# Optimization experiments

Measured on AMD Instinct MI355X. Metric: run time of the kernel, lower is better.

The kernel has to match this reference:

```python
import jax, jax.numpy as jnp
import numpy as np

N, M, C = 32768, 8192, 128
K = 3            # number of interpolation neighbors (PointNet++/RepSurf FP)
EPS_BN = 1e-5    # torch BatchNorm1d default eps
EPS_D = 1e-8     # RepSurf dist_recip eps


def setup_inputs() -> dict:
    key = jax.random.key(0)
    ks = jax.random.split(key, 16)
    s = 0.05
    inp = {
        "pos1": jax.random.normal(ks[0], (N, 3), jnp.float32),
        "pos2": jax.random.normal(ks[1], (M, 3), jnp.float32),
        "feat2": jax.random.normal(ks[2], (M, C), jnp.float32),
    }
    # MLP stack [128,128,128]: Linear + BatchNorm1d (gamma/beta) per layer
    for i in range(3):
        inp[f"W{i}"] = jax.random.normal(ks[3 + i], (C, C), jnp.float32) * s
        inp[f"b{i}"] = jnp.zeros((C,), jnp.float32)
        inp[f"g{i}"] = jnp.ones((C,), jnp.float32)
        inp[f"be{i}"] = jnp.zeros((C,), jnp.float32)
    return inp


def _lin_bn_relu(x, W, b, g, be):
    # Linear -> BatchNorm1d (training-mode batch stats, biased var) -> ReLU
    y = x @ W.T + b
    m = y.mean(axis=0)
    v = y.var(axis=0)
    return jax.nn.relu((y - m) * jax.lax.rsqrt(v + EPS_BN) * g + be)


def reference(pos1, pos2, feat2, W0, b0, g0, be0, W1, b1, g1, be1, W2, b2, g2, be2):
    # squared pairwise distances [N, M] (memory-bound: 1 GB fp32)
    d = ((pos1 ** 2).sum(-1, keepdims=True)
         + (pos2 ** 2).sum(-1)[None, :]
         - 2.0 * (pos1 @ pos2.T))
    neg_d, idx = jax.lax.top_k(-d, K)          # 3 nearest neighbors
    dk = jnp.maximum(-neg_d, 0.0)              # [N, K] squared dists
    w = 1.0 / (dk + EPS_D)
    w = w / w.sum(-1, keepdims=True)           # inverse-distance weights
    # gather neighbor features and interpolate: [N, K, C] -> [N, C]
    interp = jnp.einsum('nkc,nk->nc', feat2[idx], w)
    x = _lin_bn_relu(interp, W0, b0, g0, be0)
    x = _lin_bn_relu(x, W1, b1, g1, be1)
    x = _lin_bn_relu(x, W2, b2, g2, be2)
    return x
```

## Files before the change

### kernel.cpp

```cpp
#include <hip/hip_runtime.h>
#include <math.h>

#define NQ 32768
#define MC 8192
#define CC 128
#define EPS_BN 1e-5f
#define EPS_D  1e-8

#define DBL_BIG 1e300
#define IDX_BIG 0x7fffffff

#define QB  64
#define TB  512
#define NW  8
#define CH  2048
#define HM  (MC / 2)
#define NCH (HM / CH)
#define SLC (CH / NW)
#define KMASK 0xFFFFE000u
#define IMASK 0x1FFFu
#define NSURV 64

typedef __attribute__((ext_vector_type(8))) short bf16x8;
typedef __attribute__((ext_vector_type(4))) float floatx4;
typedef unsigned short ushort_t;

__device__ __forceinline__ unsigned umin_(unsigned a, unsigned b) { return a < b ? a : b; }
__device__ __forceinline__ unsigned umax_(unsigned a, unsigned b) { return a > b ? a : b; }

__device__ __forceinline__ unsigned bf16pair(float a, float b) {
    unsigned ua = __float_as_uint(a); ua = (ua + 0x7FFFu + ((ua >> 16) & 1u)) >> 16;
    unsigned ub = __float_as_uint(b); ub = (ub + 0x7FFFu + ((ub >> 16) & 1u)) >> 16;
    return ua | (ub << 16);
}

__global__ __launch_bounds__(TB) void knn_kernel(const float* __restrict__ pos1,
                                                 const float* __restrict__ pos2,
                                                 unsigned* __restrict__ skeys) {
    __shared__ float4 sp4[CH * 3 / 4];
    __shared__ unsigned skey[QB][NW * 4];

    const int half = blockIdx.x & 1;
    const int bq   = blockIdx.x >> 1;
    const int wv = threadIdx.x >> 6;
    const int ln = threadIdx.x & 63;
    const int q  = bq * QB + ln;

    const float px = pos1[q * 3 + 0];
    const float py = pos1[q * 3 + 1];
    const float pz = pos1[q * 3 + 2];

    unsigned k0 = 0xFFFFFFFFu, k1 = 0xFFFFFFFFu, k2 = 0xFFFFFFFFu, k3 = 0xFFFFFFFFu;

    for (int c0 = 0; c0 < NCH; ++c0) {
        const int cb = half * HM + c0 * CH;
        __syncthreads();
        {
            const float4* g4 = (const float4*)(pos2 + (size_t)cb * 3);
#pragma unroll
            for (int i = threadIdx.x; i < CH * 3 / 4; i += TB) sp4[i] = g4[i];
        }
        __syncthreads();
        const float4* b4 = sp4 + wv * (SLC * 3 / 4);
        const int jb = cb + wv * SLC;
#pragma unroll 2
        for (int gi = 0; gi < SLC / 4; ++gi) {
            const float4 A = b4[gi * 3 + 0];
            const float4 B = b4[gi * 3 + 1];
            const float4 Cv = b4[gi * 3 + 2];
            const int j = jb + gi * 4;
            const float cx[4] = {A.x, A.w, B.z, Cv.y};
            const float cy[4] = {A.y, B.x, B.w, Cv.z};
            const float cz[4] = {A.z, B.y, Cv.x, Cv.w};
#pragma unroll
            for (int u = 0; u < 4; ++u) {
                const float dx = px - cx[u], dy = py - cy[u], dz = pz - cz[u];
                const float d = fmaf(dx, dx, fmaf(dy, dy, dz * dz));
                unsigned e = (__float_as_uint(d) & KMASK) | (unsigned)(j + u);
                unsigned t;
                t = umin_(k0, e); e = umax_(k0, e); k0 = t;
                t = umin_(k1, e); e = umax_(k1, e); k1 = t;
                t = umin_(k2, e); e = umax_(k2, e); k2 = t;
                k3 = umin_(k3, e);
            }
        }
    }
    skey[ln][wv * 4 + 0] = k0;
    skey[ln][wv * 4 + 1] = k1;
    skey[ln][wv * 4 + 2] = k2;
    skey[ln][wv * 4 + 3] = k3;
    __syncthreads();

#pragma unroll
    for (int t = threadIdx.x * 4; t < threadIdx.x * 4 + 4; ++t) {
        const int ql = t >> 5, slot = t & 31;
        skeys[(size_t)((bq * QB + ql) * 2 + half) * 32 + slot] = skey[ql][slot];
    }
}

__global__ __launch_bounds__(256) void rerank_kernel(const float* __restrict__ pos1,
                                                     const float* __restrict__ pos2,
                                                     const unsigned* __restrict__ skeys,
                                                     int* __restrict__ idx3,
                                                     float* __restrict__ w3) {
    const int q = blockIdx.x * 256 + threadIdx.x;
    const double qx = (double)pos1[q * 3 + 0];
    const double qy = (double)pos1[q * 3 + 1];
    const double qz = (double)pos1[q * 3 + 2];
    double b0 = DBL_BIG, b1 = DBL_BIG, b2 = DBL_BIG;
    int    j0 = IDX_BIG, j1 = IDX_BIG, j2 = IDX_BIG;
    const uint4* kp = (const uint4*)(skeys + (size_t)q * NSURV);
#pragma unroll 4
    for (int g = 0; g < NSURV / 4; ++g) {
        const uint4 kk = kp[g];
        const unsigned ks[4] = {kk.x, kk.y, kk.z, kk.w};
#pragma unroll
        for (int u = 0; u < 4; ++u) {
            const int id = (int)(ks[u] & IMASK);
            const double x = (double)pos2[id * 3 + 0];
            const double y = (double)pos2[id * 3 + 1];
            const double z = (double)pos2[id * 3 + 2];
            const double ax = qx - x, ay = qy - y, az = qz - z;
            const double d = ax * ax + ay * ay + az * az;
            const bool l2 = (d < b2) || (d == b2 && id < j2);
            if (l2) {
                const bool l1 = (d < b1) || (d == b1 && id < j1);
                const bool l0 = (d < b0) || (d == b0 && id < j0);
                b2 = l1 ? b1 : d;              j2 = l1 ? j1 : id;
                b1 = l1 ? (l0 ? b0 : d) : b1;  j1 = l1 ? (l0 ? j0 : id) : j1;
                b0 = l0 ? d : b0;              j0 = l0 ? id : j0;
            }
        }
    }
    const double r0 = 1.0 / (fmax(b0, 0.0) + EPS_D);
    const double r1 = 1.0 / (fmax(b1, 0.0) + EPS_D);
    const double r2 = 1.0 / (fmax(b2, 0.0) + EPS_D);
    const double inv = 1.0 / (r0 + r1 + r2);
    idx3[q * 3 + 0] = j0; idx3[q * 3 + 1] = j1; idx3[q * 3 + 2] = j2;
    w3[q * 3 + 0] = (float)(r0 * inv);
    w3[q * 3 + 1] = (float)(r1 * inv);
    w3[q * 3 + 2] = (float)(r2 * inv);
}

__global__ __launch_bounds__(256) void prep_w(const float* __restrict__ W0,
                                              const float* __restrict__ W1,
                                              const float* __restrict__ W2,
                                              ushort_t* __restrict__ out) {
    const int l = blockIdx.x >> 4;
    const int i4 = ((blockIdx.x & 15) * 256 + threadIdx.x) * 4;
    const float* W = (l == 0) ? W0 : ((l == 1) ? W1 : W2);
    const float4 v = *(const float4*)&W[i4];
    unsigned* dst = (unsigned*)(out + (size_t)l * CC * CC);
    dst[(i4 >> 1) + 0] = bf16pair(v.x, v.y);
    dst[(i4 >> 1) + 1] = bf16pair(v.z, v.w);
}

template <int MODE>
__global__ __launch_bounds__(256) void gemm_mfma(const float* __restrict__ Xsrc,
                                                 const int* __restrict__ idx3,
                                                 const float* __restrict__ w3,
                                                 const float* __restrict__ scale,
                                                 const float* __restrict__ shift,
                                                 const ushort_t* __restrict__ Wb,
                                                 const float* __restrict__ bias,
                                                 float* __restrict__ Y,
                                                 float* __restrict__ partials) {
    __shared__ short xa[64][136];
    __shared__ short wb[128][136];
    __shared__ float blk_s[CC], blk_q[CC];

    const int row0 = blockIdx.x * 64;

    if (threadIdx.x < CC) { blk_s[threadIdx.x] = 0.f; blk_q[threadIdx.x] = 0.f; }

#pragma unroll
    for (int e = threadIdx.x; e < 64 * 32; e += 256) {
        const int r = e >> 5, c4 = e & 31;
        const int nrow = row0 + r;
        float4 v;
        if (MODE == 0) {
            const int i0 = idx3[nrow * 3 + 0], i1 = idx3[nrow * 3 + 1], i2 = idx3[nrow * 3 + 2];
            const float w0 = w3[nrow * 3 + 0], w1 = w3[nrow * 3 + 1], w2 = w3[nrow * 3 + 2];
            const float4 f0 = *(const float4*)&Xsrc[(size_t)i0 * CC + c4 * 4];
            const float4 f1 = *(const float4*)&Xsrc[(size_t)i1 * CC + c4 * 4];
            const float4 f2 = *(const float4*)&Xsrc[(size_t)i2 * CC + c4 * 4];
            v.x = w0 * f0.x + w1 * f1.x + w2 * f2.x;
            v.y = w0 * f0.y + w1 * f1.y + w2 * f2.y;
            v.z = w0 * f0.z + w1 * f1.z + w2 * f2.z;
            v.w = w0 * f0.w + w1 * f1.w + w2 * f2.w;
        } else {
            const float4 x  = *(const float4*)&Xsrc[(size_t)nrow * CC + c4 * 4];
            const float4 sc = *(const float4*)&scale[c4 * 4];
            const float4 sh = *(const float4*)&shift[c4 * 4];
            v.x = fmaxf(fmaf(x.x, sc.x, sh.x), 0.f);
            v.y = fmaxf(fmaf(x.y, sc.y, sh.y), 0.f);
            v.z = fmaxf(fmaf(x.z, sc.z, sh.z), 0.f);
            v.w = fmaxf(fmaf(x.w, sc.w, sh.w), 0.f);
        }
        unsigned* dst = (unsigned*)&xa[r][0];
        dst[c4 * 2 + 0] = bf16pair(v.x, v.y);
        dst[c4 * 2 + 1] = bf16pair(v.z, v.w);
    }
#pragma unroll
    for (int e = threadIdx.x; e < 128 * 16; e += 256) {
        const int co = e >> 4, seg = e & 15;
        *(float4*)&wb[co][seg * 8] = *(const float4*)&Wb[(size_t)co * CC + seg * 8];
    }
    __syncthreads();

    const int lane = threadIdx.x & 63;
    const int wv = threadIdx.x >> 6;
    const int nn = lane & 15;
    const int quad = lane >> 4;

    floatx4 acc[8] = {};

    const short* arow = &xa[wv * 16 + nn][0];
#pragma unroll
    for (int ks = 0; ks < 4; ++ks) {
        const bf16x8 a = *(const bf16x8*)(arow + ks * 32 + quad * 8);
#pragma unroll
        for (int ct = 0; ct < 8; ++ct) {
            const bf16x8 b = *(const bf16x8*)(&wb[ct * 16 + nn][0] + ks * 32 + quad * 8);
            acc[ct] = __builtin_amdgcn_mfma_f32_16x16x32_bf16(a, b, acc[ct], 0, 0, 0);
        }
    }

#pragma unroll
    for (int ct = 0; ct < 8; ++ct) {
        const float bv = bias[ct * 16 + nn];
        float s = 0.f, qv = 0.f;
#pragma unroll
        for (int r = 0; r < 4; ++r) {
            acc[ct][r] += bv;
            s += acc[ct][r];
            qv = fmaf(acc[ct][r], acc[ct][r], qv);
        }
#pragma unroll
        for (int r = 0; r < 4; ++r)
            Y[(size_t)(row0 + wv * 16 + quad * 4 + r) * CC + ct * 16 + nn] = acc[ct][r];
        s += __shfl_xor(s, 16, 64); s += __shfl_xor(s, 32, 64);
        qv += __shfl_xor(qv, 16, 64); qv += __shfl_xor(qv, 32, 64);
        if (quad == 0) {
            atomicAdd(&blk_s[ct * 16 + nn], s);
            atomicAdd(&blk_q[ct * 16 + nn], qv);
        }
    }
    __syncthreads();
    {
        const int ch = threadIdx.x;
        const float v = (ch < CC) ? blk_s[ch] : blk_q[ch - CC];
        partials[(size_t)ch * 512 + blockIdx.x] = v;
    }
}

__global__ __launch_bounds__(256) void reduce_stats(const float* __restrict__ P,
                                                    const float* __restrict__ g,
                                                    const float* __restrict__ be,
                                                    float* __restrict__ sc,
                                                    float* __restrict__ sh) {
    __shared__ float accS[4], accQ[4];
    const int c = blockIdx.x;
    const int t = threadIdx.x;
    float s  = P[(size_t)c * 512 + t]        + P[(size_t)c * 512 + 256 + t];
    float qv = P[(size_t)(c + CC) * 512 + t] + P[(size_t)(c + CC) * 512 + 256 + t];
#pragma unroll
    for (int off = 32; off >= 1; off >>= 1) {
        s  += __shfl_xor(s, off, 64);
        qv += __shfl_xor(qv, off, 64);
    }
    if ((t & 63) == 0) { accS[t >> 6] = s; accQ[t >> 6] = qv; }
    __syncthreads();
    if (t == 0) {
        const float S = accS[0] + accS[1] + accS[2] + accS[3];
        const float Q = accQ[0] + accQ[1] + accQ[2] + accQ[3];
        const float m = S * (1.f / (float)NQ);
        const float v = fmaf(-m, m, Q * (1.f / (float)NQ));
        const float rstd = rsqrtf(v + EPS_BN);
        const float scl = g[c] * rstd;
        sc[c] = scl;
        sh[c] = fmaf(-m, scl, be[c]);
    }
}

__global__ __launch_bounds__(256) void bn_relu_kernel(const float* __restrict__ Y,
                                                      const float* __restrict__ sc,
                                                      const float* __restrict__ sh,
                                                      float* __restrict__ out) {
    const int i4 = blockIdx.x * 256 + threadIdx.x;
    const int c4 = (i4 & 31) * 4;
    const float4 y = ((const float4*)Y)[i4];
    const float4 s = *(const float4*)&sc[c4];
    const float4 h = *(const float4*)&sh[c4];
    float4 o;
    o.x = fmaxf(fmaf(y.x, s.x, h.x), 0.f);
    o.y = fmaxf(fmaf(y.y, s.y, h.y), 0.f);
    o.z = fmaxf(fmaf(y.z, s.z, h.z), 0.f);
    o.w = fmaxf(fmaf(y.w, s.w, h.w), 0.f);
    ((float4*)out)[i4] = o;
}

extern "C" void kernel_launch(void* const* d_in, const int* in_sizes, int n_in,
                              void* d_out, int out_size, void* d_ws, size_t ws_size,
                              hipStream_t stream) {
    (void)in_sizes; (void)n_in; (void)out_size; (void)ws_size;

    const float* pos1  = (const float*)d_in[0];
    const float* pos2  = (const float*)d_in[1];
    const float* feat2 = (const float*)d_in[2];
    const float* Wl[3]  = {(const float*)d_in[3], (const float*)d_in[7],  (const float*)d_in[11]};
    const float* bl[3]  = {(const float*)d_in[4], (const float*)d_in[8],  (const float*)d_in[12]};
    const float* gl[3]  = {(const float*)d_in[5], (const float*)d_in[9],  (const float*)d_in[13]};
    const float* bel[3] = {(const float*)d_in[6], (const float*)d_in[10], (const float*)d_in[14]};

    float* ws = (float*)d_ws;
    float* B0   = ws;
    float* B1   = B0 + (size_t)NQ * CC;
    unsigned* skeys = (unsigned*)B1;
    int*   idx3 = (int*)(B1 + (size_t)NQ * CC);
    float* w3   = (float*)(idx3 + (size_t)NQ * 3);
    float* part = w3 + (size_t)NQ * 3;
    float* scsh = part + 256 * 512;
    ushort_t* Wbf = (ushort_t*)(scsh + 3 * 256);

    float* sc0 = scsh + 0 * 256; float* sh0 = sc0 + CC;
    float* sc1 = scsh + 1 * 256; float* sh1 = sc1 + CC;
    float* sc2 = scsh + 2 * 256; float* sh2 = sc2 + CC;

    prep_w<<<48, 256, 0, stream>>>(Wl[0], Wl[1], Wl[2], Wbf);
    knn_kernel<<<(NQ / QB) * 2, TB, 0, stream>>>(pos1, pos2, skeys);
    rerank_kernel<<<NQ / 256, 256, 0, stream>>>(pos1, pos2, skeys, idx3, w3);

    gemm_mfma<0><<<NQ / 64, 256, 0, stream>>>(feat2, idx3, w3, nullptr, nullptr,
                                              Wbf + 0 * CC * CC, bl[0], B0, part);
    reduce_stats<<<CC, 256, 0, stream>>>(part, gl[0], bel[0], sc0, sh0);
    gemm_mfma<1><<<NQ / 64, 256, 0, stream>>>(B0, nullptr, nullptr, sc0, sh0,
                                              Wbf + 1 * CC * CC, bl[1], B1, part);
    reduce_stats<<<CC, 256, 0, stream>>>(part, gl[1], bel[1], sc1, sh1);
    gemm_mfma<1><<<NQ / 64, 256, 0, stream>>>(B1, nullptr, nullptr, sc1, sh1,
                                              Wbf + 2 * CC * CC, bl[2], B0, part);
    reduce_stats<<<CC, 256, 0, stream>>>(part, gl[2], bel[2], sc2, sh2);
    bn_relu_kernel<<<(size_t)NQ * CC / 1024, 256, 0, stream>>>(B0, sc2, sh2, (float*)d_out);
}
```

Baseline: 231.7 us.

## Fuse weight prep, rerank and BN stats reduction into KNN and GEMM kernels

Weight bf16 conversion now runs in extra blocks of the KNN kernel. The distance loop uses an expanded form, with per-point squared norms precomputed into LDS as float4. The exact double-precision rerank moves into the first GEMM kernel, with four threads per query and an LDS merge. The separate reduce_stats kernels are replaced by a last-block-done atomic counter inside each GEMM, cutting the launch count roughly in half. The expanded float distance can cancel to small negative values that sort as huge keys, which risks dropping true neighbors in the coarse filter.

Measured after the change: 442.2 us. +90.9%, slower.

```diff
diff --git a/kernel.cpp b/kernel.cpp
--- a/kernel.cpp
+++ b/kernel.cpp
@@ -20,6 +20,8 @@
 #define KMASK 0xFFFFE000u
 #define IMASK 0x1FFFu
 #define NSURV 64
+#define KNN_B ((NQ / QB) * 2)
+#define GEMM_B (NQ / 64)
 
 typedef __attribute__((ext_vector_type(8))) short bf16x8;
 typedef __attribute__((ext_vector_type(4))) float floatx4;
@@ -36,9 +38,29 @@
 
 __global__ __launch_bounds__(TB) void knn_kernel(const float* __restrict__ pos1,
                                                  const float* __restrict__ pos2,
-                                                 unsigned* __restrict__ skeys) {
-    __shared__ float4 sp4[CH * 3 / 4];
+                                                 unsigned* __restrict__ skeys,
+                                                 const float* __restrict__ W0,
+                                                 const float* __restrict__ W1,
+                                                 const float* __restrict__ W2,
+                                                 ushort_t* __restrict__ Wbf,
+                                                 unsigned* __restrict__ cnt) {
+    __shared__ __align__(16) float4 sp4[CH];
     __shared__ unsigned skey[QB][NW * 4];
+
+    if (blockIdx.x >= KNN_B) {
+        const int pb = blockIdx.x - KNN_B;
+        const int f = pb * TB + threadIdx.x;
+        const float* Ws[3] = {W0, W1, W2};
+#pragma unroll
+        for (int l = 0; l < 3; ++l) {
+            const float4 v = ((const float4*)Ws[l])[f];
+            unsigned* dst = (unsigned*)(Wbf + (size_t)l * CC * CC);
+            dst[f * 2 + 0] = bf16pair(v.x, v.y);
+            dst[f * 2 + 1] = bf16pair(v.z, v.w);
+        }
+        if (pb == 0 && threadIdx.x < 4) cnt[threadIdx.x] = 0u;
+        return;
+    }
 
     const int half = blockIdx.x & 1;
     const int bq   = blockIdx.x >> 1;
@@ -49,6 +71,8 @@
     const float px = pos1[q * 3 + 0];
     const float py = pos1[q * 3 + 1];
     const float pz = pos1[q * 3 + 2];
+    const float s1 = px * px + py * py + pz * pz;
+    const float m2x = -2.f * px, m2y = -2.f * py, m2z = -2.f * pz;
 
     unsigned k0 = 0xFFFFFFFFu, k1 = 0xFFFFFFFFu, k2 = 0xFFFFFFFFu, k3 = 0xFFFFFFFFu;
 
@@ -56,33 +80,30 @@
         const int cb = half * HM + c0 * CH;
         __syncthreads();
         {
-            const float4* g4 = (const float4*)(pos2 + (size_t)cb * 3);
-#pragma unroll
-            for (int i = threadIdx.x; i < CH * 3 / 4; i += TB) sp4[i] = g4[i];
+            const float4* g = (const float4*)(pos2 + (size_t)(cb + threadIdx.x * 4) * 3);
+            const float4 f0 = g[0], f1 = g[1], f2 = g[2];
+            sp4[threadIdx.x * 4 + 0] = make_float4(f0.x, f0.y, f0.z,
+                fmaf(f0.x, f0.x, fmaf(f0.y, f0.y, f0.z * f0.z)));
+            sp4[threadIdx.x * 4 + 1] = make_float4(f0.w, f1.x, f1.y,
+                fmaf(f0.w, f0.w, fmaf(f1.x, f1.x, f1.y * f1.y)));
+            sp4[threadIdx.x * 4 + 2] = make_float4(f1.z, f1.w, f2.x,
+                fmaf(f1.z, f1.z, fmaf(f1.w, f1.w, f2.x * f2.x)));
+            sp4[threadIdx.x * 4 + 3] = make_float4(f2.y, f2.z, f2.w,
+                fmaf(f2.y, f2.y, fmaf(f2.z, f2.z, f2.w * f2.w)));
         }
         __syncthreads();
-        const float4* b4 = sp4 + wv * (SLC * 3 / 4);
+        const float4* b4 = sp4 + wv * SLC;
         const int jb = cb + wv * SLC;
-#pragma unroll 2
-        for (int gi = 0; gi < SLC / 4; ++gi) {
-            const float4 A = b4[gi * 3 + 0];
-            const float4 B = b4[gi * 3 + 1];
-            const float4 Cv = b4[gi * 3 + 2];
-            const int j = jb + gi * 4;
-            const float cx[4] = {A.x, A.w, B.z, Cv.y};
-            const float cy[4] = {A.y, B.x, B.w, Cv.z};
-            const float cz[4] = {A.z, B.y, Cv.x, Cv.w};
-#pragma unroll
-            for (int u = 0; u < 4; ++u) {
-                const float dx = px - cx[u], dy = py - cy[u], dz = pz - cz[u];
-                const float d = fmaf(dx, dx, fmaf(dy, dy, dz * dz));
-                unsigned e = (__float_as_uint(d) & KMASK) | (unsigned)(j + u);
-                unsigned t;
-                t = umin_(k0, e); e = umax_(k0, e); k0 = t;
-                t = umin_(k1, e); e = umax_(k1, e); k1 = t;
-                t = umin_(k2, e); e = umax_(k2, e); k2 = t;
-                k3 = umin_(k3, e);
-            }
+#pragma unroll 4
+        for (int e = 0; e < SLC; ++e) {
+            const float4 c = b4[e];
+            const float d = fmaf(m2x, c.x, fmaf(m2y, c.y, fmaf(m2z, c.z, c.w + s1)));
+            unsigned ek = (__float_as_uint(d) & KMASK) | (unsigned)(jb + e);
+            unsigned t;
+            t = umin_(k0, ek); ek = umax_(k0, ek); k0 = t;
+            t = umin_(k1, ek); ek = umax_(k1, ek); k1 = t;
+            t = umin_(k2, ek); ek = umax_(k2, ek); k2 = t;
+            k3 = umin_(k3, ek);
         }
     }
     skey[ln][wv * 4 + 0] = k0;
@@ -94,112 +115,138 @@
 #pragma unroll
     for (int t = threadIdx.x * 4; t < threadIdx.x * 4 + 4; ++t) {
         const int ql = t >> 5, slot = t & 31;
-        skeys[(size_t)((bq * QB + ql) * 2 + half) * 32 + slot] = skey[ql][slot];
-    }
-}
-
-__global__ __launch_bounds__(256) void rerank_kernel(const float* __restrict__ pos1,
-                                                     const float* __restrict__ pos2,
-                                                     const unsigned* __restrict__ skeys,
-                                                     int* __restrict__ idx3,
-                                                     float* __restrict__ w3) {
-    const int q = blockIdx.x * 256 + threadIdx.x;
-    const double qx = (double)pos1[q * 3 + 0];
-    const double qy = (double)pos1[q * 3 + 1];
-    const double qz = (double)pos1[q * 3 + 2];
-    double b0 = DBL_BIG, b1 = DBL_BIG, b2 = DBL_BIG;
-    int    j0 = IDX_BIG, j1 = IDX_BIG, j2 = IDX_BIG;
-    const uint4* kp = (const uint4*)(skeys + (size_t)q * NSURV);
-#pragma unroll 4
-    for (int g = 0; g < NSURV / 4; ++g) {
-        const uint4 kk = kp[g];
-        const unsigned ks[4] = {kk.x, kk.y, kk.z, kk.w};
-#pragma unroll
-        for (int u = 0; u < 4; ++u) {
-            const int id = (int)(ks[u] & IMASK);
-            const double x = (double)pos2[id * 3 + 0];
-            const double y = (double)pos2[id * 3 + 1];
-            const double z = (double)pos2[id * 3 + 2];
-            const double ax = qx - x, ay = qy - y, az = qz - z;
-            const double d = ax * ax + ay * ay + az * az;
-            const bool l2 = (d < b2) || (d == b2 && id < j2);
-            if (l2) {
-                const bool l1 = (d < b1) || (d == b1 && id < j1);
-                const bool l0 = (d < b0) || (d == b0 && id < j0);
-                b2 = l1 ? b1 : d;              j2 = l1 ? j1 : id;
-                b1 = l1 ? (l0 ? b0 : d) : b1;  j1 = l1 ? (l0 ? j0 : id) : j1;
-                b0 = l0 ? d : b0;              j0 = l0 ? id : j0;
-            }
-        }
-    }
-    const double r0 = 1.0 / (fmax(b0, 0.0) + EPS_D);
-    const double r1 = 1.0 / (fmax(b1, 0.0) + EPS_D);
-    const double r2 = 1.0 / (fmax(b2, 0.0) + EPS_D);
-    const double inv = 1.0 / (r0 + r1 + r2);
-    idx3[q * 3 + 0] = j0; idx3[q * 3 + 1] = j1; idx3[q * 3 + 2] = j2;
-    w3[q * 3 + 0] = (float)(r0 * inv);
-    w3[q * 3 + 1] = (float)(r1 * inv);
-    w3[q * 3 + 2] = (float)(r2 * inv);
-}
-
-__global__ __launch_bounds__(256) void prep_w(const float* __restrict__ W0,
-                                              const float* __restrict__ W1,
-                                              const float* __restrict__ W2,
-                                              ushort_t* __restrict__ out) {
-    const int l = blockIdx.x >> 4;
-    const int i4 = ((blockIdx.x & 15) * 256 + threadIdx.x) * 4;
-    const float* W = (l == 0) ? W0 : ((l == 1) ? W1 : W2);
-    const float4 v = *(const float4*)&W[i4];
-    unsigned* dst = (unsigned*)(out + (size_t)l * CC * CC);
-    dst[(i4 >> 1) + 0] = bf16pair(v.x, v.y);
-    dst[(i4 >> 1) + 1] = bf16pair(v.z, v.w);
+        skeys[(size_t)(bq * QB + ql) * NSURV + half * 32 + slot] = skey[ql][slot];
+    }
 }
 
 template <int MODE>
 __global__ __launch_bounds__(256) void gemm_mfma(const float* __restrict__ Xsrc,
-                                                 const int* __restrict__ idx3,
-                                                 const float* __restrict__ w3,
-                                                 const float* __restrict__ scale,
-                                                 const float* __restrict__ shift,
+                                                 const unsigned* __restrict__ skeys,
+                                                 const float* __restrict__ pos1,
+                                                 const float* __restrict__ pos2,
+                                                 const float* __restrict__ scaleIn,
+                                                 const float* __restrict__ shiftIn,
                                                  const ushort_t* __restrict__ Wb,
                                                  const float* __restrict__ bias,
+                                                 const float* __restrict__ g,
+                                                 const float* __restrict__ be,
                                                  float* __restrict__ Y,
-                                                 float* __restrict__ partials) {
-    __shared__ short xa[64][136];
-    __shared__ short wb[128][136];
+                                                 float* __restrict__ partials,
+                                                 unsigned* __restrict__ cnt,
+                                                 float* __restrict__ scOut,
+                                                 float* __restrict__ shOut) {
+    __shared__ __align__(16) short xa[64][136];
+    __shared__ __align__(16) short wb[128][136];
     __shared__ float blk_s[CC], blk_q[CC];
+    __shared__ int lastFlag;
 
     const int row0 = blockIdx.x * 64;
 
-    if (threadIdx.x < CC) { blk_s[threadIdx.x] = 0.f; blk_q[threadIdx.x] = 0.f; }
-
-#pragma unroll
-    for (int e = threadIdx.x; e < 64 * 32; e += 256) {
-        const int r = e >> 5, c4 = e & 31;
-        const int nrow = row0 + r;
-        float4 v;
-        if (MODE == 0) {
-            const int i0 = idx3[nrow * 3 + 0], i1 = idx3[nrow * 3 + 1], i2 = idx3[nrow * 3 + 2];
-            const float w0 = w3[nrow * 3 + 0], w1 = w3[nrow * 3 + 1], w2 = w3[nrow * 3 + 2];
+    if constexpr (MODE == 0) {
+        __shared__ int   lidx[QB][3];
+        __shared__ float lw[QB][3];
+        {
+            double* rrd = (double*)&xa[0][0];
+            int*    rri = (int*)&wb[0][0];
+            const int ql = threadIdx.x >> 2;
+            const int pp = threadIdx.x & 3;
+            const int qg = row0 + ql;
+            const double qx = (double)pos1[qg * 3 + 0];
+            const double qy = (double)pos1[qg * 3 + 1];
+            const double qz = (double)pos1[qg * 3 + 2];
+            double b0 = DBL_BIG, b1 = DBL_BIG, b2 = DBL_BIG;
+            int    j0 = IDX_BIG, j1 = IDX_BIG, j2 = IDX_BIG;
+            const uint4* kp = (const uint4*)(skeys + (size_t)qg * NSURV + pp * 16);
+#pragma unroll
+            for (int gi = 0; gi < 4; ++gi) {
+                const uint4 kk = kp[gi];
+                const unsigned ks[4] = {kk.x, kk.y, kk.z, kk.w};
+#pragma unroll
+                for (int u = 0; u < 4; ++u) {
+                    const int id = (int)(ks[u] & IMASK);
+                    const double x = (double)pos2[id * 3 + 0];
+                    const double y = (double)pos2[id * 3 + 1];
+                    const double z = (double)pos2[id * 3 + 2];
+                    const double ax = qx - x, ay = qy - y, az = qz - z;
+                    const double d = ax * ax + ay * ay + az * az;
+                    const bool l2 = (d < b2) || (d == b2 && id < j2);
+                    if (l2) {
+                        const bool l1 = (d < b1) || (d == b1 && id < j1);
+                        const bool l0 = (d < b0) || (d == b0 && id < j0);
+                        b2 = l1 ? b1 : d;              j2 = l1 ? j1 : id;
+                        b1 = l1 ? (l0 ? b0 : d) : b1;  j1 = l1 ? (l0 ? j0 : id) : j1;
+                        b0 = l0 ? d : b0;              j0 = l0 ? id : j0;
+                    }
+                }
+            }
+            const int base = (ql * 4 + pp) * 3;
+            rrd[base + 0] = b0; rri[base + 0] = j0;
+            rrd[base + 1] = b1; rri[base + 1] = j1;
+            rrd[base + 2] = b2; rri[base + 2] = j2;
+            __syncthreads();
+            if (threadIdx.x < QB) {
+                const int qq = threadIdx.x;
+                double c0 = DBL_BIG, c1 = DBL_BIG, c2 = DBL_BIG;
+                int    i0 = IDX_BIG, i1 = IDX_BIG, i2 = IDX_BIG;
+#pragma unroll
+                for (int s = 0; s < 12; ++s) {
+                    const double d = rrd[qq * 12 + s];
+                    const int   id = rri[qq * 12 + s];
+                    const bool l2 = (d < c2) || (d == c2 && id < i2);
+                    if (l2) {
+                        const bool l1 = (d < c1) || (d == c1 && id < i1);
+                        const bool l0 = (d < c0) || (d == c0 && id < i0);
+                        c2 = l1 ? c1 : d;              i2 = l1 ? i1 : id;
+                        c1 = l1 ? (l0 ? c0 : d) : c1;  i1 = l1 ? (l0 ? i0 : id) : i1;
+                        c0 = l0 ? d : c0;              i0 = l0 ? id : i0;
+                    }
+                }
+                const double r0 = 1.0 / (c0 + EPS_D);
+                const double r1 = 1.0 / (c1 + EPS_D);
+                const double r2 = 1.0 / (c2 + EPS_D);
+                const double inv = 1.0 / (r0 + r1 + r2);
+                lidx[qq][0] = i0; lidx[qq][1] = i1; lidx[qq][2] = i2;
+                lw[qq][0] = (float)(r0 * inv);
+                lw[qq][1] = (float)(r1 * inv);
+                lw[qq][2] = (float)(r2 * inv);
+            }
+            __syncthreads();
+        }
+        if (threadIdx.x < CC) { blk_s[threadIdx.x] = 0.f; blk_q[threadIdx.x] = 0.f; }
+#pragma unroll
+        for (int e = threadIdx.x; e < 64 * 32; e += 256) {
+            const int r = e >> 5, c4 = e & 31;
+            const int i0 = lidx[r][0], i1 = lidx[r][1], i2 = lidx[r][2];
+            const float w0 = lw[r][0], w1 = lw[r][1], w2 = lw[r][2];
             const float4 f0 = *(const float4*)&Xsrc[(size_t)i0 * CC + c4 * 4];
             const float4 f1 = *(const float4*)&Xsrc[(size_t)i1 * CC + c4 * 4];
             const float4 f2 = *(const float4*)&Xsrc[(size_t)i2 * CC + c4 * 4];
+            float4 v;
             v.x = w0 * f0.x + w1 * f1.x + w2 * f2.x;
             v.y = w0 * f0.y + w1 * f1.y + w2 * f2.y;
             v.z = w0 * f0.z + w1 * f1.z + w2 * f2.z;
             v.w = w0 * f0.w + w1 * f1.w + w2 * f2.w;
-        } else {
-            const float4 x  = *(const float4*)&Xsrc[(size_t)nrow * CC + c4 * 4];
-            const float4 sc = *(const float4*)&scale[c4 * 4];
-            const float4 sh = *(const float4*)&shift[c4 * 4];
+            unsigned* dst = (unsigned*)&xa[r][0];
+            dst[c4 * 2 + 0] = bf16pair(v.x, v.y);
+            dst[c4 * 2 + 1] = bf16pair(v.z, v.w);
+        }
+    } else {
+        if (threadIdx.x < CC) { blk_s[threadIdx.x] = 0.f; blk_q[threadIdx.x] = 0.f; }
+#pragma unroll
+        for (int e = threadIdx.x; e < 64 * 32; e += 256) {
+            const int r = e >> 5, c4 = e & 31;
+            const float4 x  = *(const float4*)&Xsrc[(size_t)(row0 + r) * CC + c4 * 4];
+            const float4 sc = *(const float4*)&scaleIn[c4 * 4];
+            const float4 sh = *(const float4*)&shiftIn[c4 * 4];
+            float4 v;
             v.x = fmaxf(fmaf(x.x, sc.x, sh.x), 0.f);
             v.y = fmaxf(fmaf(x.y, sc.y, sh.y), 0.f);
             v.z = fmaxf(fmaf(x.z, sc.z, sh.z), 0.f);
             v.w = fmaxf(fmaf(x.w, sc.w, sh.w), 0.f);
-        }
-        unsigned* dst = (unsigned*)&xa[r][0];
-        dst[c4 * 2 + 0] = bf16pair(v.x, v.y);
-        dst[c4 * 2 + 1] = bf16pair(v.z, v.w);
+            unsigned* dst = (unsigned*)&xa[r][0];
+            dst[c4 * 2 + 0] = bf16pair(v.x, v.y);
+            dst[c4 * 2 + 1] = bf16pair(v.z, v.w);
+        }
     }
 #pragma unroll
     for (int e = threadIdx.x; e < 128 * 16; e += 256) {
@@ -250,36 +297,33 @@
     {
         const int ch = threadIdx.x;
         const float v = (ch < CC) ? blk_s[ch] : blk_q[ch - CC];
-        partials[(size_t)ch * 512 + blockIdx.x] = v;
-    }
-}
-
-__global__ __launch_bounds__(256) void reduce_stats(const float* __restrict__ P,
-                                                    const float* __restrict__ g,
-                                                    const float* __restrict__ be,
-                                                    float* __restrict__ sc,
-                                                    float* __restrict__ sh) {
-    __shared__ float accS[4], accQ[4];
-    const int c = blockIdx.x;
-    const int t = threadIdx.x;
-    float s  = P[(size_t)c * 512 + t]        + P[(size_t)c * 512 + 256 + t];
-    float qv = P[(size_t)(c + CC) * 512 + t] + P[(size_t)(c + CC) * 512 + 256 + t];
-#pragma unroll
-    for (int off = 32; off >= 1; off >>= 1) {
-        s  += __shfl_xor(s, off, 64);
-        qv += __shfl_xor(qv, off, 64);
-    }
-    if ((t & 63) == 0) { accS[t >> 6] = s; accQ[t >> 6] = qv; }
-    __syncthreads();
-    if (t == 0) {
-        const float S = accS[0] + accS[1] + accS[2] + accS[3];
-        const float Q = accQ[0] + accQ[1] + accQ[2] + accQ[3];
-        const float m = S * (1.f / (float)NQ);
-        const float v = fmaf(-m, m, Q * (1.f / (float)NQ));
-        const float rstd = rsqrtf(v + EPS_BN);
-        const float scl = g[c] * rstd;
-        sc[c] = scl;
-        sh[c] = fmaf(-m, scl, be[c]);
+        __hip_atomic_store(&partials[(size_t)ch * GEMM_B + blockIdx.x], v,
+                           __ATOMIC_RELAXED, __HIP_MEMORY_SCOPE_AGENT);
+    }
+    __syncthreads();
+    if (threadIdx.x == 0) {
+        const unsigned old = __hip_atomic_fetch_add(cnt, 1u, __ATOMIC_ACQ_REL,
+                                                    __HIP_MEMORY_SCOPE_AGENT);
+        lastFlag = (old == (unsigned)(gridDim.x - 1)) ? 1 : 0;
+    }
+    __syncthreads();
+    if (lastFlag) {
+        const int t = threadIdx.x;
+        float tot = 0.f;
+        const float* row = partials + (size_t)t * GEMM_B;
+#pragma unroll 8
+        for (int i = 0; i < GEMM_B; ++i)
+            tot += __hip_atomic_load(&row[i], __ATOMIC_RELAXED, __HIP_MEMORY_SCOPE_AGENT);
+        if (t < CC) blk_s[t] = tot; else blk_q[t - CC] = tot;
+        __syncthreads();
+        if (t < CC) {
+            const float m = blk_s[t] * (1.f / (float)NQ);
+            const float v = fmaf(-m, m, blk_q[t] * (1.f / (float)NQ));
+            const float rstd = rsqrtf(v + EPS_BN);
+            const float scl = g[t] * rstd;
+            scOut[t] = scl;
+            shOut[t] = fmaf(-m, scl, be[t]);
+        }
     }
 }
 
@@ -317,28 +361,28 @@
     float* B0   = ws;
     float* B1   = B0 + (size_t)NQ * CC;
     unsigned* skeys = (unsigned*)B1;
-    int*   idx3 = (int*)(B1 + (size_t)NQ * CC);
-    float* w3   = (float*)(idx3 + (size_t)NQ * 3);
-    float* part = w3 + (size_t)NQ * 3;
-    float* scsh = part + 256 * 512;
+    float* part = B1 + (size_t)NQ * CC;
+    float* scsh = part + 256 * GEMM_B;
     ushort_t* Wbf = (ushort_t*)(scsh + 3 * 256);
+    unsigned* cnt = (unsigned*)(Wbf + 3 * CC * CC);
 
     float* sc0 = scsh + 0 * 256; float* sh0 = sc0 + CC;
     float* sc1 = scsh + 1 * 256; float* sh1 = sc1 + CC;
     float* sc2 = scsh + 2 * 256; float* sh2 = sc2 + CC;
 
-    prep_w<<<48, 256, 0, stream>>>(Wl[0], Wl[1], Wl[2], Wbf);
-    knn_kernel<<<(NQ / QB) * 2, TB, 0, stream>>>(pos1, pos2, skeys);
-    rerank_kernel<<<NQ / 256, 256, 0, stream>>>(pos1, pos2, skeys, idx3, w3);
-
-    gemm_mfma<0><<<NQ / 64, 256, 0, stream>>>(feat2, idx3, w3, nullptr, nullptr,
-                                              Wbf + 0 * CC * CC, bl[0], B0, part);
-    reduce_stats<<<CC, 256, 0, stream>>>(part, gl[0], bel[0], sc0, sh0);
-    gemm_mfma<1><<<NQ / 64, 256, 0, stream>>>(B0, nullptr, nullptr, sc0, sh0,
-                                              Wbf + 1 * CC * CC, bl[1], B1, part);
-    reduce_stats<<<CC, 256, 0, stream>>>(part, gl[1], bel[1], sc1, sh1);
-    gemm_mfma<1><<<NQ / 64, 256, 0, stream>>>(B1, nullptr, nullptr, sc1, sh1,
-                                              Wbf + 2 * CC * CC, bl[2], B0, part);
-    reduce_stats<<<CC, 256, 0, stream>>>(part, gl[2], bel[2], sc2, sh2);
+    knn_kernel<<<KNN_B + 8, TB, 0, stream>>>(pos1, pos2, skeys,
+                                             Wl[0], Wl[1], Wl[2], Wbf, cnt);
+    gemm_mfma<0><<<GEMM_B, 256, 0, stream>>>(feat2, skeys, pos1, pos2,
+                                             nullptr, nullptr,
+                                             Wbf + 0 * CC * CC, bl[0], gl[0], bel[0],
+                                             B0, part, cnt + 0, sc0, sh0);
+    gemm_mfma<1><<<GEMM_B, 256, 0, stream>>>(B0, nullptr, nullptr, nullptr,
+                                             sc0, sh0,
+                                             Wbf + 1 * CC * CC, bl[1], gl[1], bel[1],
+                                             B1, part, cnt + 1, sc1, sh1);
+    gemm_mfma<1><<<GEMM_B, 256, 0, stream>>>(B1, nullptr, nullptr, nullptr,
+                                             sc1, sh1,
+                                             Wbf + 2 * CC * CC, bl[2], gl[2], bel[2],
+                                             B0, part, cnt + 2, sc2, sh2);
     bn_relu_kernel<<<(size_t)NQ * CC / 1024, 256, 0, stream>>>(B0, sc2, sh2, (float*)d_out);
 }
```
